# Kernel tuning notes

Hardware: AMD Instinct MI355X
Metric: run time of the kernel (lower is better)

## Reference

```python
import jax, jax.numpy as jnp
import numpy as np

H = 128
NG, NS, NP = 50000, 20000, 30000
NUM_PC_FEATURES = 5
EPS = 1e-12


def seg_sum(x, idx, n):
    return jax.ops.segment_sum(x, idx, num_segments=n)


def seg_mean(x, idx, n):
    s = seg_sum(x, idx, n)
    cnt = seg_sum(jnp.ones((x.shape[0],), x.dtype), idx, n)
    return s / jnp.maximum(cnt, 1.0)[:, None]


def gcn_norm(row, col, n, add_self_loops):
    deg = seg_sum(jnp.ones(row.shape, jnp.float32), col, n)
    if add_self_loops:
        deg = deg + 1.0
    dinv = jnp.where(deg > 0, deg ** -0.5, 0.0)
    return dinv[row] * dinv[col], dinv


def tag_conv(x, row, col, n, Ws, b):
    # TAGConv: out = sum_k (A_hat^k x) W_k + b, symmetric norm, no self loops
    norm, _ = gcn_norm(row, col, n, False)
    out = x @ Ws[0]
    h = x
    for k in range(1, Ws.shape[0]):
        h = seg_sum(norm[:, None] * h[row], col, n)
        out = out + h @ Ws[k]
    return out + b


def rgcn_conv(x, row, col, etype, n, W, root, b):
    # RGCNConv: per-relation mean aggregation + root transform
    h = jnp.einsum('nc,rcd->rnd', x, W)  # [R, N, H]
    msg = h[etype, row]                  # [E, H]
    cnt = jnp.zeros((n, W.shape[0]), x.dtype).at[col, etype].add(1.0)
    w = 1.0 / jnp.maximum(cnt[col, etype], 1.0)
    return seg_sum(msg * w[:, None], col, n) + x @ root + b


def gcn_layer(x, row, col, n, W, b):
    # GCNConv: self loops + symmetric normalization
    xW = x @ W
    norm, dinv = gcn_norm(row, col, n, True)
    return seg_sum(norm[:, None] * xW[row], col, n) + (dinv ** 2)[:, None] * xW + b


def sage_conv(xs, xd, row, col, nd, lw, lb, rw):
    # SAGEConv with mean aggregation, root weight, L2 output normalization
    m = seg_mean(xs[row], col, nd)
    out = m @ lw + lb + xd @ rw
    nrm = jnp.maximum(jnp.linalg.norm(out, axis=-1, keepdims=True), EPS)
    return out / nrm


def setup_inputs() -> dict:
    key = jax.random.key(0)
    ks = iter(jax.random.split(key, 64))

    def nrm(shape):
        return jax.random.normal(next(ks), shape, jnp.float32) * 0.05

    def edges(ns, nd, e):
        return jnp.stack([jax.random.randint(next(ks), (e,), 0, ns, jnp.int32),
                          jax.random.randint(next(ks), (e,), 0, nd, jnp.int32)])

    return dict(
        game_x=nrm((NG, 7)),
        state_x=nrm((NS, 6)),
        pc_x=nrm((NP, NUM_PC_FEATURES)),
        edge_index_v_v=edges(NG, NG, 500000),
        edge_type_v_v=jax.random.randint(next(ks), (500000,), 0, 3, jnp.int32),
        edge_index_history_v_s=edges(NG, NS, 300000),
        edge_attr_history_v_s=nrm((300000, 2)),
        edge_index_in_v_s=edges(NG, NS, 300000),
        edge_index_s_s=edges(NS, NS, 200000),
        edge_index_pc_pc=edges(NP, NP, 300000),
        edge_index_pc_state=edges(NP, NS, 200000),
        edge_index_state_pc=edges(NS, NP, 100000),
        tag10_w=nrm((4, 7, H)), tag10_b=nrm((H,)),
        rgcn_w=nrm((3, H, H)), rgcn_root=nrm((H, H)), rgcn_b=nrm((H,)),
        gcn1_w=nrm((NUM_PC_FEATURES, H)), gcn1_b=nrm((H,)),
        gcn2_w=nrm((H, H)), gcn2_b=nrm((H,)),
        rg_key_w=nrm((6, H)), rg_key_b=nrm((H,)),
        rg_query_w=nrm((H, H)), rg_query_b=nrm((H,)),
        rg_value_w=nrm((H, H)), rg_value_b=nrm((H,)),
        rg_edge_w=nrm((2, H)), rg_skip_w=nrm((6, H)), rg_b=nrm((H,)),
        sage32_lw=nrm((H, H)), sage32_lb=nrm((H,)), sage32_rw=nrm((H, H)),
        sage4_lw=nrm((H, H)), sage4_lb=nrm((H,)), sage4_rw=nrm((H, H)),
        sage42_lw=nrm((H, H)), sage42_lb=nrm((H,)), sage42_rw=nrm((H, H)),
        pcs_lw=nrm((H, H)), pcs_lb=nrm((H,)), pcs_rw=nrm((H, H)),
        tag2_w=nrm((3, H, H)), tag2_b=nrm((H,)),
        sage5_lw=nrm((H, H)), sage5_lb=nrm((H,)), sage5_rw=nrm((H, H)),
        lin_w=nrm((H, 32)), lin_b=nrm((32,)),
        linl_w=nrm((32, 1)), linl_b=nrm((1,)),
    )


def reference(game_x, state_x, pc_x, edge_index_v_v, edge_type_v_v,
              edge_index_history_v_s, edge_attr_history_v_s, edge_index_in_v_s,
              edge_index_s_s, edge_index_pc_pc, edge_index_pc_state, edge_index_state_pc,
              tag10_w, tag10_b, rgcn_w, rgcn_root, rgcn_b,
              gcn1_w, gcn1_b, gcn2_w, gcn2_b,
              rg_key_w, rg_key_b, rg_query_w, rg_query_b, rg_value_w, rg_value_b,
              rg_edge_w, rg_skip_w, rg_b,
              sage32_lw, sage32_lb, sage32_rw,
              sage4_lw, sage4_lb, sage4_rw,
              sage42_lw, sage42_lb, sage42_rw,
              pcs_lw, pcs_lb, pcs_rw,
              tag2_w, tag2_b,
              sage5_lw, sage5_lb, sage5_rw,
              lin_w, lin_b, linl_w, linl_b):
    relu = jax.nn.relu
    rvv, cvv = edge_index_v_v[0], edge_index_v_v[1]
    g = relu(tag_conv(game_x, rvv, cvv, NG, tag10_w, tag10_b))
    g = relu(rgcn_conv(g, rvv, cvv, edge_type_v_v, NG, rgcn_w, rgcn_root, rgcn_b))
    rp, cp = edge_index_pc_pc[0], edge_index_pc_pc[1]
    p = relu(gcn_layer(pc_x, rp, cp, NP, gcn1_w, gcn1_b))
    p = relu(gcn_layer(p, rp, cp, NP, gcn2_w, gcn2_b))
    rh, ch = edge_index_history_v_s[0], edge_index_history_v_s[1]
    # ResGatedGraphConv((game, state), H, edge_dim=2)
    kk = state_x @ rg_key_w + rg_key_b
    q = g @ rg_query_w + rg_query_b
    v = g @ rg_value_w + rg_value_b
    e = edge_attr_history_v_s @ rg_edge_w
    eta = jax.nn.sigmoid(kk[ch] + q[rh] + e)
    s = relu(seg_sum(eta * v[rh], ch, NS) + state_x @ rg_skip_w + rg_b)
    s = relu(sage_conv(g, s, rh, ch, NS, sage32_lw, sage32_lb, sage32_rw))
    ri, ci = edge_index_in_v_s[0], edge_index_in_v_s[1]
    s = relu(sage_conv(g, s, ri, ci, NS, sage4_lw, sage4_lb, sage4_rw))
    s = relu(sage_conv(g, s, ri, ci, NS, sage42_lw, sage42_lb, sage42_rw))
    rps, cps = edge_index_pc_state[0], edge_index_pc_state[1]
    s = relu(sage_conv(p, s, rps, cps, NS, pcs_lw, pcs_lb, pcs_rw))
    rs, cs = edge_index_s_s[0], edge_index_s_s[1]
    s = relu(tag_conv(s, rs, cs, NS, tag2_w, tag2_b))
    s = relu(sage_conv(s, s, rs, cs, NS, sage5_lw, sage5_lb, sage5_rw))
    s = relu(s @ lin_w + lin_b)
    return jax.nn.log_softmax(s @ linl_w + linl_b, axis=0)
```

## Files before the change

kernel.cpp:

```cpp
#include <hip/hip_runtime.h>
#include <cstdint>

#define H 128
static const int NG = 50000, NS = 20000, NP = 30000;

#define TG_RELU 2
#define TG_NORM 4
#define TG_OUTBF16 8

#define CSR_CHUNK 8192

typedef __attribute__((ext_vector_type(8))) short bf16x8;
typedef __attribute__((ext_vector_type(4))) float f32x4;
typedef __attribute__((ext_vector_type(2))) float v2f;

static inline int nblk(long long n) { return (int)((n + 255) / 256); }

__device__ inline unsigned short f2b(float f) {
  unsigned int u = __float_as_uint(f);
  u += 0x7FFFu + ((u >> 16) & 1u);
  return (unsigned short)(u >> 16);
}
__device__ inline float b2f(unsigned short u) {
  return __uint_as_float(((unsigned int)u) << 16);
}
__device__ inline float2 bfp2(unsigned int u) {
  return make_float2(__uint_as_float(u << 16), __uint_as_float(u & 0xFFFF0000u));
}
__device__ inline unsigned int f2bfp(float x, float y) {
  return ((unsigned int)f2b(y) << 16) | (unsigned int)f2b(x);
}
__device__ inline float2 f8p2(unsigned short u) {
  v2f r = __builtin_amdgcn_cvt_pk_f32_fp8((int)(unsigned int)u, false);
  return make_float2(r.x, r.y);
}
__device__ inline unsigned char f2f8(float x) {
  int r = __builtin_amdgcn_cvt_pk_fp8_f32(x, 0.f, 0, false);
  return (unsigned char)(r & 0xFF);
}

struct Seg6 {
  const int* col[6];
  const int* row[6];
  const int* et0;
  int nodeoff[7];
  int edgeoff[7];
  int mode[6];
  float addself[6];
  int hasdinv[6];
};

__global__ __launch_bounds__(256) void k_hist(Seg6 sg, int EE, int* __restrict__ table) {
  __shared__ int h[512];
  int tid = threadIdx.x, blk = blockIdx.x;
  h[tid] = 0; h[tid + 256] = 0;
  __syncthreads();
  int e0 = blk * CSR_CHUNK, e1 = min(EE, e0 + CSR_CHUNK);
  for (int e = e0 + tid; e < e1; e += 256) {
    int gi = 0;
    while (e >= sg.edgeoff[gi + 1]) gi++;
    int le = e - sg.edgeoff[gi];
    int gn = sg.nodeoff[gi] + sg.col[gi][le];
    atomicAdd(&h[gn >> 9], 1);
  }
  __syncthreads();
  table[blk * 512 + tid] = h[tid];
  table[blk * 512 + tid + 256] = h[tid + 256];
}

__global__ void k_scanT(int* __restrict__ table, int nblkA, int* __restrict__ coarseOff) {
  int b = threadIdx.x;
  int s = 0;
  for (int k = 0; k < nblkA; k++) s += table[k * 512 + b];
  __shared__ int cs[512];
  cs[b] = s;
  __syncthreads();
  for (int off = 1; off < 512; off <<= 1) {
    int v = cs[b];
    int u = (b >= off) ? cs[b - off] : 0;
    __syncthreads();
    cs[b] = v + u;
    __syncthreads();
  }
  int excl = (b > 0) ? cs[b - 1] : 0;
  coarseOff[b] = excl;
  if (b == 511) coarseOff[512] = cs[511];
  int run = excl;
  for (int k = 0; k < nblkA; k++) {
    int t = table[k * 512 + b];
    table[k * 512 + b] = run;
    run += t;
  }
}

__global__ __launch_bounds__(256) void k_scatterA(Seg6 sg, int EE, const int* __restrict__ table,
                                                  uint2* __restrict__ tmp) {
  __shared__ int cur[512];
  int tid = threadIdx.x, blk = blockIdx.x;
  cur[tid] = table[blk * 512 + tid];
  cur[tid + 256] = table[blk * 512 + tid + 256];
  __syncthreads();
  int e0 = blk * CSR_CHUNK, e1 = min(EE, e0 + CSR_CHUNK);
  for (int e = e0 + tid; e < e1; e += 256) {
    int gi = 0;
    while (e >= sg.edgeoff[gi + 1]) gi++;
    int le = e - sg.edgeoff[gi];
    int gn = sg.nodeoff[gi] + sg.col[gi][le];
    int m = sg.mode[gi];
    int pay;
    if (m == 2) pay = le;
    else {
      pay = sg.row[gi][le];
      if (m == 1) pay |= sg.et0[le] << 16;
    }
    int pos = atomicAdd(&cur[gn >> 9], 1);
    tmp[pos] = make_uint2((unsigned)gn, (unsigned)pay);
  }
}

__global__ __launch_bounds__(256) void k_localCSR(const uint2* __restrict__ tmp,
                                                  const int* __restrict__ coarseOff,
                                                  Seg6 sg, int NN, int EE, int B,
                                                  int* __restrict__ rowptr,
                                                  int* __restrict__ eidx,
                                                  float* __restrict__ dinv) {
  int b = blockIdx.x, tid = threadIdx.x;
  int base = b * 512;
  int nNodes = min(512, NN - base);
  int beg = coarseOff[b], end = coarseOff[b + 1];
  __shared__ int cnt[512];
  __shared__ int off[512];
  __shared__ int ps[256];
  cnt[tid] = 0; cnt[tid + 256] = 0;
  __syncthreads();
  for (int j = beg + tid; j < end; j += 256)
    atomicAdd(&cnt[tmp[j].x - base], 1);
  __syncthreads();
  int a = cnt[2 * tid], bb = cnt[2 * tid + 1];
  ps[tid] = a + bb;
  __syncthreads();
  for (int o = 1; o < 256; o <<= 1) {
    int v = ps[tid];
    int u = (tid >= o) ? ps[tid - o] : 0;
    __syncthreads();
    ps[tid] = v + u;
    __syncthreads();
  }
  int excl = (tid > 0) ? ps[tid - 1] : 0;
  off[2 * tid] = excl;
  off[2 * tid + 1] = excl + a;
  __syncthreads();
  for (int i = tid; i < nNodes; i += 256) {
    int gid = base + i;
    rowptr[gid] = beg + off[i];
    int gi = 0;
    while (gid >= sg.nodeoff[gi + 1]) gi++;
    if (sg.hasdinv[gi]) {
      float d = (float)cnt[i] + sg.addself[gi];
      dinv[gid] = (d > 0.f) ? rsqrtf(d) : 0.f;
    }
  }
  if (b == B - 1 && tid == 0) rowptr[NN] = EE;
  __syncthreads();
  for (int j = beg + tid; j < end; j += 256) {
    uint2 p = tmp[j];
    int pos = beg + atomicAdd(&off[p.x - base], 1);
    eidx[pos] = (int)p.y;
  }
}

struct PackD { const float* src; int Ksrc; int Kdst; };
struct Pack17 { PackD d[17]; int koff[18]; };

__global__ void k_pack(Pack17 p, unsigned short* __restrict__ Wt, int totalRows) {
  int t = blockIdx.x * blockDim.x + threadIdx.x;
  if (t >= totalRows * 128) return;
  int gk = t >> 7, n = t & 127;
  int w = 0;
  while (gk >= p.koff[w + 1]) w++;
  int k = gk - p.koff[w];
  float v = (k < p.d[w].Ksrc) ? p.d[w].src[(size_t)k * 128 + n] : 0.f;
  Wt[(size_t)p.koff[w] * 128 + (size_t)n * p.d[w].Kdst + k] = f2b(v);
}

__global__ __launch_bounds__(256) void k_gmean(const unsigned short* __restrict__ src,
                                               const int* __restrict__ eidx,
                                               const int* __restrict__ rowptr,
                                               unsigned short* __restrict__ out, int N) {
  int c = blockIdx.x * 4 + (threadIdx.x >> 6);
  if (c >= N) return;
  int lane = threadIdx.x & 63;
  int beg = rowptr[c], end = rowptr[c + 1];
  float2 A0 = {0.f, 0.f}, A1 = {0.f, 0.f}, A2 = {0.f, 0.f}, A3 = {0.f, 0.f};
  int j = beg;
  for (; j + 4 <= end; j += 4) {
    int e0 = eidx[j], e1 = eidx[j + 1], e2 = eidx[j + 2], e3 = eidx[j + 3];
    float2 v0 = bfp2(*(const unsigned int*)(src + (size_t)e0 * H + lane * 2));
    float2 v1 = bfp2(*(const unsigned int*)(src + (size_t)e1 * H + lane * 2));
    float2 v2 = bfp2(*(const unsigned int*)(src + (size_t)e2 * H + lane * 2));
    float2 v3 = bfp2(*(const unsigned int*)(src + (size_t)e3 * H + lane * 2));
    A0.x += v0.x; A0.y += v0.y;
    A1.x += v1.x; A1.y += v1.y;
    A2.x += v2.x; A2.y += v2.y;
    A3.x += v3.x; A3.y += v3.y;
  }
  for (; j < end; j++) {
    float2 v = bfp2(*(const unsigned int*)(src + (size_t)eidx[j] * H + lane * 2));
    A0.x += v.x; A0.y += v.y;
  }
  int cnt = end - beg;
  float s = 1.f / (float)(cnt > 0 ? cnt : 1);
  float ox = (A0.x + A1.x + A2.x + A3.x) * s;
  float oy = (A0.y + A1.y + A2.y + A3.y) * s;
  *(unsigned int*)(out + (size_t)c * H + lane * 2) = f2bfp(ox, oy);
}

__global__ __launch_bounds__(256) void k_gmean_f8(const unsigned char* __restrict__ src,
                                                  const int* __restrict__ eidx,
                                                  const int* __restrict__ rowptr,
                                                  unsigned short* __restrict__ out, int N) {
  int c = blockIdx.x * 4 + (threadIdx.x >> 6);
  if (c >= N) return;
  int lane = threadIdx.x & 63;
  int beg = rowptr[c], end = rowptr[c + 1];
  float2 A0 = {0.f, 0.f}, A1 = {0.f, 0.f}, A2 = {0.f, 0.f}, A3 = {0.f, 0.f};
  int j = beg;
  for (; j + 4 <= end; j += 4) {
    int e0 = eidx[j], e1 = eidx[j + 1], e2 = eidx[j + 2], e3 = eidx[j + 3];
    float2 v0 = f8p2(*(const unsigned short*)(src + (size_t)e0 * H + lane * 2));
    float2 v1 = f8p2(*(const unsigned short*)(src + (size_t)e1 * H + lane * 2));
    float2 v2 = f8p2(*(const unsigned short*)(src + (size_t)e2 * H + lane * 2));
    float2 v3 = f8p2(*(const unsigned short*)(src + (size_t)e3 * H + lane * 2));
    A0.x += v0.x; A0.y += v0.y;
    A1.x += v1.x; A1.y += v1.y;
    A2.x += v2.x; A2.y += v2.y;
    A3.x += v3.x; A3.y += v3.y;
  }
  for (; j < end; j++) {
    float2 v = f8p2(*(const unsigned short*)(src + (size_t)eidx[j] * H + lane * 2));
    A0.x += v.x; A0.y += v.y;
  }
  int cnt = end - beg;
  float s = 1.f / (float)(cnt > 0 ? cnt : 1);
  float ox = (A0.x + A1.x + A2.x + A3.x) * s;
  float oy = (A0.y + A1.y + A2.y + A3.y) * s;
  *(unsigned int*)(out + (size_t)c * H + lane * 2) = f2bfp(ox, oy);
}

__global__ __launch_bounds__(256) void k_grel3(const unsigned char* __restrict__ src,
                                               const int* __restrict__ eidx,
                                               const int* __restrict__ rowptr,
                                               unsigned short* __restrict__ G3, int N) {
  int c = blockIdx.x * 4 + (threadIdx.x >> 6);
  if (c >= N) return;
  int lane = threadIdx.x & 63;
  int beg = rowptr[c], end = rowptr[c + 1];
  float2 a0 = {0.f, 0.f}, a1 = {0.f, 0.f}, a2 = {0.f, 0.f};
  int c0 = 0, c1 = 0, c2 = 0;
  for (int j = beg; j < end; j++) {
    int pk = eidx[j];
    int rel = pk >> 16;
    float2 v = f8p2(*(const unsigned short*)(src + (size_t)(pk & 0xFFFF) * H + lane * 2));
    if (rel == 0) { a0.x += v.x; a0.y += v.y; c0++; }
    else if (rel == 1) { a1.x += v.x; a1.y += v.y; c1++; }
    else { a2.x += v.x; a2.y += v.y; c2++; }
  }
  float s0 = 1.f / (float)(c0 > 0 ? c0 : 1);
  float s1 = 1.f / (float)(c1 > 0 ? c1 : 1);
  float s2 = 1.f / (float)(c2 > 0 ? c2 : 1);
  size_t base = (size_t)c * 384 + lane * 2;
  *(unsigned int*)(G3 + base) = f2bfp(a0.x * s0, a0.y * s0);
  *(unsigned int*)(G3 + base + 128) = f2bfp(a1.x * s1, a1.y * s1);
  *(unsigned int*)(G3 + base + 256) = f2bfp(a2.x * s2, a2.y * s2);
}

__global__ __launch_bounds__(256) void k_gnorm(const unsigned short* __restrict__ src,
                                               long ldS, int offS,
                                               const int* __restrict__ eidx,
                                               const int* __restrict__ rowptr,
                                               const float* __restrict__ dinv,
                                               const unsigned short* __restrict__ selfX,
                                               const float* __restrict__ bias,
                                               unsigned short* __restrict__ out,
                                               long ldD, int offD, int relu, int N) {
  int c = blockIdx.x * 4 + (threadIdx.x >> 6);
  if (c >= N) return;
  int lane = threadIdx.x & 63;
  int beg = rowptr[c], end = rowptr[c + 1];
  float2 A0 = {0.f, 0.f}, A1 = {0.f, 0.f}, A2 = {0.f, 0.f}, A3 = {0.f, 0.f};
  int j = beg;
  for (; j + 4 <= end; j += 4) {
    int e0 = eidx[j], e1 = eidx[j + 1], e2 = eidx[j + 2], e3 = eidx[j + 3];
    float w0 = dinv[e0], w1 = dinv[e1], w2 = dinv[e2], w3 = dinv[e3];
    float2 v0 = bfp2(*(const unsigned int*)(src + (size_t)e0 * ldS + offS + lane * 2));
    float2 v1 = bfp2(*(const unsigned int*)(src + (size_t)e1 * ldS + offS + lane * 2));
    float2 v2 = bfp2(*(const unsigned int*)(src + (size_t)e2 * ldS + offS + lane * 2));
    float2 v3 = bfp2(*(const unsigned int*)(src + (size_t)e3 * ldS + offS + lane * 2));
    A0.x = fmaf(w0, v0.x, A0.x); A0.y = fmaf(w0, v0.y, A0.y);
    A1.x = fmaf(w1, v1.x, A1.x); A1.y = fmaf(w1, v1.y, A1.y);
    A2.x = fmaf(w2, v2.x, A2.x); A2.y = fmaf(w2, v2.y, A2.y);
    A3.x = fmaf(w3, v3.x, A3.x); A3.y = fmaf(w3, v3.y, A3.y);
  }
  for (; j < end; j++) {
    int e = eidx[j];
    float w = dinv[e];
    float2 v = bfp2(*(const unsigned int*)(src + (size_t)e * ldS + offS + lane * 2));
    A0.x = fmaf(w, v.x, A0.x); A0.y = fmaf(w, v.y, A0.y);
  }
  float dc = dinv[c];
  float ox = (A0.x + A1.x + A2.x + A3.x) * dc;
  float oy = (A0.y + A1.y + A2.y + A3.y) * dc;
  if (selfX) {
    float2 sv = bfp2(*(const unsigned int*)(selfX + (size_t)c * H + lane * 2));
    ox += dc * dc * sv.x;
    oy += dc * dc * sv.y;
  }
  if (bias) {
    float2 bv = *(const float2*)(bias + lane * 2);
    ox += bv.x; oy += bv.y;
  }
  if (relu) { ox = fmaxf(ox, 0.f); oy = fmaxf(oy, 0.f); }
  *(unsigned int*)(out + (size_t)c * ldD + offD + lane * 2) = f2bfp(ox, oy);
}

__global__ __launch_bounds__(256) void k_resgated_mean(const unsigned short* __restrict__ kk,
                                                       const unsigned char* __restrict__ q,
                                                       const unsigned char* __restrict__ v,
                                                       const unsigned char* __restrict__ g,
                                                       const float* __restrict__ ea,
                                                       const float* __restrict__ We,
                                                       const int* __restrict__ rh,
                                                       const int* __restrict__ eidx,
                                                       const int* __restrict__ rowptr,
                                                       const float* __restrict__ sx,
                                                       const float* __restrict__ Wsk,
                                                       const float* __restrict__ rgb,
                                                       unsigned short* __restrict__ outS,
                                                       unsigned short* __restrict__ outM, int N) {
  int c = blockIdx.x * 4 + (threadIdx.x >> 6);
  if (c >= N) return;
  int lane = threadIdx.x & 63;
  int d0 = lane * 2;
  int beg = rowptr[c], end = rowptr[c + 1];
  float2 kload = bfp2(*(const unsigned int*)(kk + (size_t)c * H + d0));
  float2 we0 = make_float2(We[d0], We[d0 + 1]);
  float2 we1 = make_float2(We[H + d0], We[H + d0 + 1]);
  float2 accS = {0.f, 0.f}, accM = {0.f, 0.f};
  for (int j = beg; j < end; j++) {
    int e = eidx[j];
    int r = rh[e];
    float a0 = ea[2 * e], a1 = ea[2 * e + 1];
    float2 qv = f8p2(*(const unsigned short*)(q + (size_t)r * H + d0));
    float2 vv = f8p2(*(const unsigned short*)(v + (size_t)r * H + d0));
    float2 gv = f8p2(*(const unsigned short*)(g + (size_t)r * H + d0));
    float x0 = kload.x + qv.x + a0 * we0.x + a1 * we1.x;
    float x1 = kload.y + qv.y + a0 * we0.y + a1 * we1.y;
    float eta0 = 1.f / (1.f + __expf(-x0));
    float eta1 = 1.f / (1.f + __expf(-x1));
    accS.x = fmaf(eta0, vv.x, accS.x);
    accS.y = fmaf(eta1, vv.y, accS.y);
    accM.x += gv.x; accM.y += gv.y;
  }
  float sk0 = rgb[d0], sk1 = rgb[d0 + 1];
#pragma unroll
  for (int f = 0; f < 6; f++) {
    float xf = sx[c * 6 + f];
    sk0 = fmaf(xf, Wsk[f * H + d0], sk0);
    sk1 = fmaf(xf, Wsk[f * H + d0 + 1], sk1);
  }
  *(unsigned int*)(outS + (size_t)c * H + d0) =
      f2bfp(fmaxf(accS.x + sk0, 0.f), fmaxf(accS.y + sk1, 0.f));
  int cnt = end - beg;
  float s = 1.f / (float)(cnt > 0 ? cnt : 1);
  *(unsigned int*)(outM + (size_t)c * H + d0) = f2bfp(accM.x * s, accM.y * s);
}

__global__ void k_gather_norm7(const unsigned short* __restrict__ src, int ldS, int offS,
                               const int* __restrict__ eidx, const int* __restrict__ rowptr,
                               const float* __restrict__ dinv, unsigned short* __restrict__ dst,
                               int ldD, int offD) {
  int c = blockIdx.x;
  int t = threadIdx.x;
  int f = t & 7, j = t >> 3;
  int beg = rowptr[c], end = rowptr[c + 1];
  __shared__ int si[64];
  __shared__ float sw[64];
  __shared__ float red[8][8];
  float acc = 0.f;
  for (int j0 = beg; j0 < end; j0 += 64) {
    int nn = min(64, end - j0);
    __syncthreads();
    if (t < nn) {
      int r = eidx[j0 + t] & 0xFFFF;
      si[t] = r;
      sw[t] = dinv[r];
    }
    __syncthreads();
    if (f < 7)
      for (int u = j; u < nn; u += 8) acc += sw[u] * b2f(src[(size_t)si[u] * ldS + offS + f]);
  }
  red[j][f] = acc;
  __syncthreads();
  if (j == 0 && f < 7) {
    float s = 0.f;
    for (int u = 0; u < 8; u++) s += red[u][f];
    dst[(size_t)c * ldD + offD + f] = f2b(s * dinv[c]);
  }
}

__global__ void k_copy7b(const float* __restrict__ src, unsigned short* __restrict__ dst, int n) {
  long long t = (long long)blockIdx.x * blockDim.x + threadIdx.x;
  int i = (int)(t >> 3), f = (int)(t & 7);
  if (i < n && f < 7) dst[(size_t)i * 32 + f] = f2b(src[(size_t)i * 7 + f]);
}

__global__ void k_gemm128b(const float* __restrict__ X, const float* __restrict__ W,
                           const float* __restrict__ b, unsigned short* __restrict__ out,
                           int M, int K) {
  long long t = (long long)blockIdx.x * blockDim.x + threadIdx.x;
  if (t >= (long long)M * H) return;
  int i = (int)(t >> 7), h = (int)(t & 127);
  float acc = b ? b[h] : 0.f;
  const float* x = X + (long long)i * K;
  for (int k = 0; k < K; k++) acc = fmaf(x[k], W[k * H + h], acc);
  out[t] = f2b(acc);
}

__global__ __launch_bounds__(256) void k_mgemm(const unsigned short* __restrict__ X1, int ldX1, int K1,
                                               const unsigned short* __restrict__ W1t,
                                               const unsigned short* __restrict__ X2, int ldX2, int K2,
                                               const unsigned short* __restrict__ W2t,
                                               const float* __restrict__ bias,
                                               void* __restrict__ Cv, long ldC,
                                               int M, int flags,
                                               unsigned char* __restrict__ C8) {
  __shared__ unsigned short Als[64 * 40];
  __shared__ unsigned short Bls[128 * 40];
  __shared__ float rs[2][64];
  int tid = threadIdx.x;
  int lane = tid & 63, wv = tid >> 6;
  int m = lane & 15, q = lane >> 4;
  int rbase = (wv & 1) * 32;
  int cbase = (wv >> 1) * 64;
  int blockRow = blockIdx.x * 64;
  int sr = tid >> 2, skc = (tid & 3) * 8;
  f32x4 acc[2][4];
#pragma unroll
  for (int a = 0; a < 2; a++)
#pragma unroll
    for (int b = 0; b < 4; b++) acc[a][b] = (f32x4){0.f, 0.f, 0.f, 0.f};

  int Ktot = K1 + K2;
  for (int k0 = 0; k0 < Ktot; k0 += 32) {
    const unsigned short* Xb;
    const unsigned short* Wt_;
    int kr, ldx, Kw;
    if (k0 < K1) { Xb = X1; Wt_ = W1t; kr = k0; ldx = ldX1; Kw = K1; }
    else { Xb = X2; Wt_ = W2t; kr = k0 - K1; ldx = ldX2; Kw = K2; }
    __syncthreads();
    {
      int gr = blockRow + sr;
      bf16x8 xv = (bf16x8){0, 0, 0, 0, 0, 0, 0, 0};
      if (gr < M) xv = *(const bf16x8*)(Xb + (size_t)gr * ldx + kr + skc);
      *(bf16x8*)&Als[sr * 40 + skc] = xv;
    }
#pragma unroll
    for (int it = 0; it < 2; it++) {
      int fid = it * 256 + tid;
      int n = fid >> 2, kc = (fid & 3) * 8;
      *(bf16x8*)&Bls[n * 40 + kc] = *(const bf16x8*)(Wt_ + (size_t)n * Kw + kr + kc);
    }
    __syncthreads();
    bf16x8 a0 = *(const bf16x8*)&Als[(rbase + m) * 40 + q * 8];
    bf16x8 a1 = *(const bf16x8*)&Als[(rbase + 16 + m) * 40 + q * 8];
    bf16x8 b0 = *(const bf16x8*)&Bls[(cbase + m) * 40 + q * 8];
    bf16x8 b1 = *(const bf16x8*)&Bls[(cbase + 16 + m) * 40 + q * 8];
    bf16x8 b2 = *(const bf16x8*)&Bls[(cbase + 32 + m) * 40 + q * 8];
    bf16x8 b3 = *(const bf16x8*)&Bls[(cbase + 48 + m) * 40 + q * 8];
    acc[0][0] = __builtin_amdgcn_mfma_f32_16x16x32_bf16(a0, b0, acc[0][0], 0, 0, 0);
    acc[0][1] = __builtin_amdgcn_mfma_f32_16x16x32_bf16(a0, b1, acc[0][1], 0, 0, 0);
    acc[0][2] = __builtin_amdgcn_mfma_f32_16x16x32_bf16(a0, b2, acc[0][2], 0, 0, 0);
    acc[0][3] = __builtin_amdgcn_mfma_f32_16x16x32_bf16(a0, b3, acc[0][3], 0, 0, 0);
    acc[1][0] = __builtin_amdgcn_mfma_f32_16x16x32_bf16(a1, b0, acc[1][0], 0, 0, 0);
    acc[1][1] = __builtin_amdgcn_mfma_f32_16x16x32_bf16(a1, b1, acc[1][1], 0, 0, 0);
    acc[1][2] = __builtin_amdgcn_mfma_f32_16x16x32_bf16(a1, b2, acc[1][2], 0, 0, 0);
    acc[1][3] = __builtin_amdgcn_mfma_f32_16x16x32_bf16(a1, b3, acc[1][3], 0, 0, 0);
  }
  float ov[2][4][4];
  float bcol[4] = {0.f, 0.f, 0.f, 0.f};
  if (bias) {
#pragma unroll
    for (int j = 0; j < 4; j++) bcol[j] = bias[cbase + j * 16 + m];
  }
#pragma unroll
  for (int a = 0; a < 2; a++)
#pragma unroll
    for (int j = 0; j < 4; j++)
#pragma unroll
      for (int i = 0; i < 4; i++) ov[a][j][i] = acc[a][j][i] + bcol[j];

  if (flags & TG_NORM) {
#pragma unroll
    for (int a = 0; a < 2; a++)
#pragma unroll
      for (int i = 0; i < 4; i++) {
        float p = 0.f;
#pragma unroll
        for (int j = 0; j < 4; j++) p = fmaf(ov[a][j][i], ov[a][j][i], p);
        p += __shfl_xor(p, 1);
        p += __shfl_xor(p, 2);
        p += __shfl_xor(p, 4);
        p += __shfl_xor(p, 8);
        if (m == 0) rs[wv >> 1][rbase + a * 16 + q * 4 + i] = p;
      }
    __syncthreads();
#pragma unroll
    for (int a = 0; a < 2; a++)
#pragma unroll
      for (int i = 0; i < 4; i++) {
        int ridx = rbase + a * 16 + q * 4 + i;
        float s = rs[0][ridx] + rs[1][ridx];
        float f = 1.f / fmaxf(sqrtf(s), 1e-12f);
#pragma unroll
        for (int j = 0; j < 4; j++) ov[a][j][i] = fmaxf(ov[a][j][i] * f, 0.f);
      }
  } else if (flags & TG_RELU) {
#pragma unroll
    for (int a = 0; a < 2; a++)
#pragma unroll
      for (int j = 0; j < 4; j++)
#pragma unroll
        for (int i = 0; i < 4; i++) ov[a][j][i] = fmaxf(ov[a][j][i], 0.f);
  }
  if (flags & TG_OUTBF16) {
    unsigned short* C = (unsigned short*)Cv;
#pragma unroll
    for (int a = 0; a < 2; a++)
#pragma unroll
      for (int i = 0; i < 4; i++) {
        int row = blockRow + rbase + a * 16 + q * 4 + i;
        if (row < M) {
#pragma unroll
          for (int j = 0; j < 4; j++)
            C[(size_t)row * ldC + cbase + j * 16 + m] = f2b(ov[a][j][i]);
        }
      }
  } else {
    float* C = (float*)Cv;
#pragma unroll
    for (int a = 0; a < 2; a++)
#pragma unroll
      for (int i = 0; i < 4; i++) {
        int row = blockRow + rbase + a * 16 + q * 4 + i;
        if (row < M) {
#pragma unroll
          for (int j = 0; j < 4; j++)
            C[(size_t)row * ldC + cbase + j * 16 + m] = ov[a][j][i];
        }
      }
  }
  if (C8) {
#pragma unroll
    for (int a = 0; a < 2; a++)
#pragma unroll
      for (int i = 0; i < 4; i++) {
        int row = blockRow + rbase + a * 16 + q * 4 + i;
        if (row < M) {
#pragma unroll
          for (int j = 0; j < 4; j++)
            C8[(size_t)row * ldC + cbase + j * 16 + m] = f2f8(ov[a][j][i]);
        }
      }
  }
}

static inline int mgb(int M) { return (M + 63) / 64; }

__global__ __launch_bounds__(256) void k_head(const float* __restrict__ X,
                                              const float* __restrict__ lw,
                                              const float* __restrict__ lb,
                                              const float* __restrict__ lwl,
                                              const float* __restrict__ lbl,
                                              float* __restrict__ z, int M) {
  __shared__ float Wl[128 * 32];
  __shared__ float Xs[8][128];
  int tid = threadIdx.x;
  for (int i = tid * 4; i < 4096; i += 1024) *(float4*)&Wl[i] = *(const float4*)&lw[i];
  int rowBase = blockIdx.x * 8;
  {
    int idx = tid * 4;
    int xr = idx >> 7, xc = idx & 127;
    int grow = rowBase + xr;
    float4 v = make_float4(0.f, 0.f, 0.f, 0.f);
    if (grow < M) v = *(const float4*)(X + (size_t)grow * H + xc);
    *(float4*)&Xs[xr][xc] = v;
  }
  __syncthreads();
  int r = tid >> 5, o = tid & 31;
  float acc = lb[o];
  for (int k = 0; k < 128; k++) acc = fmaf(Xs[r][k], Wl[k * 32 + o], acc);
  acc = fmaxf(acc, 0.f) * lwl[o];
  for (int s = 16; s > 0; s >>= 1) acc += __shfl_down(acc, s, 32);
  int grow = rowBase + r;
  if (o == 0 && grow < M) z[grow] = acc + lbl[0];
}

__global__ void k_logsoftmax(const float* __restrict__ z, float* __restrict__ out, int n) {
  __shared__ float red[256];
  int tid = threadIdx.x;
  float m = -1e30f;
  for (int i = tid; i < n; i += 256) m = fmaxf(m, z[i]);
  red[tid] = m;
  __syncthreads();
  for (int s = 128; s > 0; s >>= 1) {
    if (tid < s) red[tid] = fmaxf(red[tid], red[tid + s]);
    __syncthreads();
  }
  float mx = red[0];
  __syncthreads();
  float sum = 0.f;
  for (int i = tid; i < n; i += 256) sum += __expf(z[i] - mx);
  red[tid] = sum;
  __syncthreads();
  for (int s = 128; s > 0; s >>= 1) {
    if (tid < s) red[tid] += red[tid + s];
    __syncthreads();
  }
  float lse = mx + logf(red[0]);
  for (int i = tid; i < n; i += 256) out[i] = z[i] - lse;
}

extern "C" void kernel_launch(void* const* d_in, const int* in_sizes, int n_in,
                              void* d_out, int out_size, void* d_ws, size_t ws_size,
                              hipStream_t stream) {
  const float* game_x = (const float*)d_in[0];
  const float* state_x = (const float*)d_in[1];
  const float* pc_x = (const float*)d_in[2];
  const int* ei_vv = (const int*)d_in[3];
  const int* et_vv = (const int*)d_in[4];
  const int* ei_hist = (const int*)d_in[5];
  const float* ea_hist = (const float*)d_in[6];
  const int* ei_in = (const int*)d_in[7];
  const int* ei_ss = (const int*)d_in[8];
  const int* ei_pp = (const int*)d_in[9];
  const int* ei_ps = (const int*)d_in[10];
  const float* tag10_w = (const float*)d_in[12];
  const float* tag10_b = (const float*)d_in[13];
  const float* rgcn_w = (const float*)d_in[14];
  const float* rgcn_root = (const float*)d_in[15];
  const float* rgcn_b = (const float*)d_in[16];
  const float* gcn1_w = (const float*)d_in[17];
  const float* gcn1_b = (const float*)d_in[18];
  const float* gcn2_w = (const float*)d_in[19];
  const float* gcn2_b = (const float*)d_in[20];
  const float* rg_key_w = (const float*)d_in[21];
  const float* rg_key_b = (const float*)d_in[22];
  const float* rg_query_w = (const float*)d_in[23];
  const float* rg_query_b = (const float*)d_in[24];
  const float* rg_value_w = (const float*)d_in[25];
  const float* rg_value_b = (const float*)d_in[26];
  const float* rg_edge_w = (const float*)d_in[27];
  const float* rg_skip_w = (const float*)d_in[28];
  const float* rg_b = (const float*)d_in[29];
  const float* sage32_lw = (const float*)d_in[30];
  const float* sage32_lb = (const float*)d_in[31];
  const float* sage32_rw = (const float*)d_in[32];
  const float* sage4_lw = (const float*)d_in[33];
  const float* sage4_lb = (const float*)d_in[34];
  const float* sage4_rw = (const float*)d_in[35];
  const float* sage42_lw = (const float*)d_in[36];
  const float* sage42_lb = (const float*)d_in[37];
  const float* sage42_rw = (const float*)d_in[38];
  const float* pcs_lw = (const float*)d_in[39];
  const float* pcs_lb = (const float*)d_in[40];
  const float* pcs_rw = (const float*)d_in[41];
  const float* tag2_w = (const float*)d_in[42];
  const float* tag2_b = (const float*)d_in[43];
  const float* sage5_lw = (const float*)d_in[44];
  const float* sage5_lb = (const float*)d_in[45];
  const float* sage5_rw = (const float*)d_in[46];
  const float* lin_w = (const float*)d_in[47];
  const float* lin_b = (const float*)d_in[48];
  const float* linl_w = (const float*)d_in[49];
  const float* linl_b = (const float*)d_in[50];

  const int Evv = in_sizes[3] / 2, Eh = in_sizes[5] / 2, Ein = in_sizes[7] / 2,
            Ess = in_sizes[8] / 2, Epp = in_sizes[9] / 2, Eps = in_sizes[10] / 2;
  const int EE = Evv + Epp + Eh + Ein + Eps + Ess;
  const int NN = NG + NP + 4 * NS;

  char* base = (char*)d_ws;
  const size_t B_NGH = (size_t)NG * H * 2;
  const size_t B_NPH = (size_t)NP * H * 2;
  const size_t B_NSH = (size_t)NS * H * 2;
  unsigned short* g_tag_b = (unsigned short*)base;
  unsigned short* g_b = (unsigned short*)(base + B_NGH);
  char* C0 = base + 2 * B_NGH;
  uint2* tmp_pairs = (uint2*)C0;
  unsigned short* P_tag10_b = (unsigned short*)C0;
  unsigned short* G3_b = (unsigned short*)C0;
  unsigned short* xW_b = (unsigned short*)C0;
  unsigned short* p1b_b = (unsigned short*)(C0 + B_NPH);
  unsigned short* p2b_b = (unsigned short*)(C0 + 2 * B_NPH);
  unsigned short* v_b = (unsigned short*)C0;
  unsigned short* q_b = g_tag_b;
  unsigned short* P_tag2_b = (unsigned short*)C0;
  char* S0 = base + 2 * B_NGH + 46000000;
  unsigned short* S_a_b = (unsigned short*)S0;
  unsigned short* S_b_b = (unsigned short*)(S0 + B_NSH);
  unsigned short* m_buf_b = (unsigned short*)(S0 + 2 * B_NSH);
  unsigned short* kk_b = (unsigned short*)(S0 + 3 * B_NSH);
  float* Sfin = (float*)(S0 + 4 * B_NSH);
  unsigned short* Wt = (unsigned short*)(S0 + 4 * B_NSH + (size_t)NS * H * 4);
  int* ip = (int*)(S0 + 4 * B_NSH + (size_t)NS * H * 4 + 700000);
  int* rp_all = ip; ip += NN + 1;
  int* eidx_all = ip; ip += EE;
  int* table = ip; ip += 512 * 240;
  int* coarseOff = ip; ip += 520;
  float* fp = (float*)ip;
  float* dinv_all = fp; fp += NN;
  float* z = fp; fp += NS;
  unsigned char* g_tag_8 = (unsigned char*)(z + NS);
  unsigned char* g_8 = g_tag_8 + (size_t)NG * H;
  unsigned char* q_8 = g_8 + (size_t)NG * H;
  unsigned char* v_8 = q_8 + (size_t)NG * H;

  Seg6 sg;
  sg.col[0] = ei_vv + Evv;  sg.row[0] = ei_vv;
  sg.col[1] = ei_pp + Epp;  sg.row[1] = ei_pp;
  sg.col[2] = ei_hist + Eh; sg.row[2] = ei_hist;
  sg.col[3] = ei_in + Ein;  sg.row[3] = ei_in;
  sg.col[4] = ei_ps + Eps;  sg.row[4] = ei_ps;
  sg.col[5] = ei_ss + Ess;  sg.row[5] = ei_ss;
  sg.et0 = et_vv;
  int no[7] = {0, NG, NG + NP, NG + NP + NS, NG + NP + 2 * NS, NG + NP + 3 * NS, NN};
  int eo[7] = {0, Evv, Evv + Epp, Evv + Epp + Eh, Evv + Epp + Eh + Ein,
               Evv + Epp + Eh + Ein + Eps, EE};
  for (int i = 0; i < 7; i++) { sg.nodeoff[i] = no[i]; sg.edgeoff[i] = eo[i]; }
  int md[6] = {1, 0, 2, 0, 0, 0};
  float as[6] = {0.f, 1.f, 0.f, 0.f, 0.f, 0.f};
  int hd[6] = {1, 1, 0, 0, 0, 1};
  for (int i = 0; i < 6; i++) { sg.mode[i] = md[i]; sg.addself[i] = as[i]; sg.hasdinv[i] = hd[i]; }

  const int* rp_vv = rp_all + no[0];
  const int* rp_pp = rp_all + no[1];
  const int* rp_hh = rp_all + no[2];
  const int* rp_in = rp_all + no[3];
  const int* rp_ps = rp_all + no[4];
  const int* rp_ss = rp_all + no[5];
  const float* dinvG = dinv_all + no[0];
  const float* dinvP = dinv_all + no[1];
  const float* dinvS = dinv_all + no[5];
  const int* rh = ei_hist;

  Pack17 pk;
  const float* wsrc[17] = {tag10_w, rgcn_w, rgcn_root, gcn2_w, rg_query_w, rg_value_w,
                           sage32_lw, sage32_rw, sage4_lw, sage4_rw, sage42_lw, sage42_rw,
                           pcs_lw, pcs_rw, tag2_w, sage5_lw, sage5_rw};
  int ksrc[17] = {28, 384, 128, 128, 128, 128, 128, 128, 128, 128, 128, 128, 128, 128, 384, 128, 128};
  int kdst[17] = {32, 384, 128, 128, 128, 128, 128, 128, 128, 128, 128, 128, 128, 128, 384, 128, 128};
  int run = 0;
  for (int i = 0; i < 17; i++) {
    pk.d[i].src = wsrc[i]; pk.d[i].Ksrc = ksrc[i]; pk.d[i].Kdst = kdst[i];
    pk.koff[i] = run; run += kdst[i];
  }
  pk.koff[17] = run;
  unsigned short* WT[17];
  for (int i = 0; i < 17; i++) WT[i] = Wt + (size_t)pk.koff[i] * 128;
  k_pack<<<nblk((long long)run * 128), 256, 0, stream>>>(pk, Wt, run);

  int nblkA = (EE + CSR_CHUNK - 1) / CSR_CHUNK;
  int B = (NN + 511) / 512;
  k_hist<<<nblkA, 256, 0, stream>>>(sg, EE, table);
  k_scanT<<<1, 512, 0, stream>>>(table, nblkA, coarseOff);
  k_scatterA<<<nblkA, 256, 0, stream>>>(sg, EE, table, tmp_pairs);
  k_localCSR<<<B, 256, 0, stream>>>(tmp_pairs, coarseOff, sg, NN, EE, B,
                                    rp_all, eidx_all, dinv_all);

  hipMemsetAsync(P_tag10_b, 0, (size_t)NG * 32 * 2, stream);
  k_copy7b<<<nblk((long long)NG * 8), 256, 0, stream>>>(game_x, P_tag10_b, NG);
  k_gather_norm7<<<NG, 64, 0, stream>>>(P_tag10_b, 32, 0, eidx_all, rp_vv, dinvG, P_tag10_b, 32, 7);
  k_gather_norm7<<<NG, 64, 0, stream>>>(P_tag10_b, 32, 7, eidx_all, rp_vv, dinvG, P_tag10_b, 32, 14);
  k_gather_norm7<<<NG, 64, 0, stream>>>(P_tag10_b, 32, 14, eidx_all, rp_vv, dinvG, P_tag10_b, 32, 21);
  k_mgemm<<<mgb(NG), 256, 0, stream>>>(P_tag10_b, 32, 32, WT[0], nullptr, 0, 0, nullptr,
                                       tag10_b, g_tag_b, H, NG, TG_RELU | TG_OUTBF16, g_tag_8);

  k_grel3<<<(NG + 3) / 4, 256, 0, stream>>>(g_tag_8, eidx_all, rp_vv, G3_b, NG);
  k_mgemm<<<mgb(NG), 256, 0, stream>>>(G3_b, 384, 384, WT[1], g_tag_b, H, H, WT[2],
                                       rgcn_b, g_b, H, NG, TG_RELU | TG_OUTBF16, g_8);

  k_gemm128b<<<nblk((long long)NP * H), 256, 0, stream>>>(pc_x, gcn1_w, nullptr, xW_b, NP, 5);
  k_gnorm<<<(NP + 3) / 4, 256, 0, stream>>>(xW_b, H, 0, eidx_all, rp_pp, dinvP, xW_b, gcn1_b,
                                            p1b_b, H, 0, 1, NP);
  k_mgemm<<<mgb(NP), 256, 0, stream>>>(p1b_b, H, H, WT[3], nullptr, 0, 0, nullptr,
                                       nullptr, xW_b, H, NP, TG_OUTBF16, nullptr);
  k_gnorm<<<(NP + 3) / 4, 256, 0, stream>>>(xW_b, H, 0, eidx_all, rp_pp, dinvP, xW_b, gcn2_b,
                                            p2b_b, H, 0, 1, NP);

  k_gemm128b<<<nblk((long long)NS * H), 256, 0, stream>>>(state_x, rg_key_w, rg_key_b, kk_b, NS, 6);
  k_mgemm<<<mgb(NG), 256, 0, stream>>>(g_b, H, H, WT[4], nullptr, 0, 0, nullptr,
                                       rg_query_b, q_b, H, NG, TG_OUTBF16, q_8);
  k_mgemm<<<mgb(NG), 256, 0, stream>>>(g_b, H, H, WT[5], nullptr, 0, 0, nullptr,
                                       rg_value_b, v_b, H, NG, TG_OUTBF16, v_8);
  k_resgated_mean<<<(NS + 3) / 4, 256, 0, stream>>>(kk_b, q_8, v_8, g_8, ea_hist, rg_edge_w, rh,
                                                    eidx_all, rp_hh, state_x, rg_skip_w, rg_b,
                                                    S_a_b, m_buf_b, NS);

  k_mgemm<<<mgb(NS), 256, 0, stream>>>(m_buf_b, H, H, WT[6], S_a_b, H, H, WT[7],
                                       sage32_lb, S_b_b, H, NS, TG_NORM | TG_OUTBF16, nullptr);

  k_gmean_f8<<<(NS + 3) / 4, 256, 0, stream>>>(g_8, eidx_all, rp_in, m_buf_b, NS);
  k_mgemm<<<mgb(NS), 256, 0, stream>>>(m_buf_b, H, H, WT[8], S_b_b, H, H, WT[9],
                                       sage4_lb, S_a_b, H, NS, TG_NORM | TG_OUTBF16, nullptr);
  k_mgemm<<<mgb(NS), 256, 0, stream>>>(m_buf_b, H, H, WT[10], S_a_b, H, H, WT[11],
                                       sage42_lb, S_b_b, H, NS, TG_NORM | TG_OUTBF16, nullptr);

  k_gmean<<<(NS + 3) / 4, 256, 0, stream>>>(p2b_b, eidx_all, rp_ps, m_buf_b, NS);
  k_mgemm<<<mgb(NS), 256, 0, stream>>>(m_buf_b, H, H, WT[12], S_b_b, H, H, WT[13],
                                       pcs_lb, P_tag2_b, 384, NS, TG_NORM | TG_OUTBF16, nullptr);

  k_gnorm<<<(NS + 3) / 4, 256, 0, stream>>>(P_tag2_b, 384, 0, eidx_all, rp_ss, dinvS, nullptr,
                                            nullptr, P_tag2_b, 384, 128, 0, NS);
  k_gnorm<<<(NS + 3) / 4, 256, 0, stream>>>(P_tag2_b, 384, 128, eidx_all, rp_ss, dinvS, nullptr,
                                            nullptr, P_tag2_b, 384, 256, 0, NS);
  k_mgemm<<<mgb(NS), 256, 0, stream>>>(P_tag2_b, 384, 384, WT[14], nullptr, 0, 0, nullptr,
                                       tag2_b, S_b_b, H, NS, TG_RELU | TG_OUTBF16, nullptr);

  k_gmean<<<(NS + 3) / 4, 256, 0, stream>>>(S_b_b, eidx_all, rp_ss, m_buf_b, NS);
  k_mgemm<<<mgb(NS), 256, 0, stream>>>(m_buf_b, H, H, WT[15], S_b_b, H, H, WT[16],
                                       sage5_lb, Sfin, H, NS, TG_NORM, nullptr);

  k_head<<<(NS + 7) / 8, 256, 0, stream>>>(Sfin, lin_w, lin_b, linl_w, linl_b, z, NS);
  k_logsoftmax<<<1, 256, 0, stream>>>(z, (float*)d_out, NS);
}
```

Measured before the change: 806.9 us.

## Unroll gather loops by four and use wave-per-node 7-wide TAG gather

```diff
diff --git a/kernel.cpp b/kernel.cpp
--- a/kernel.cpp
+++ b/kernel.cpp
@@ -257,7 +257,28 @@
   int beg = rowptr[c], end = rowptr[c + 1];
   float2 a0 = {0.f, 0.f}, a1 = {0.f, 0.f}, a2 = {0.f, 0.f};
   int c0 = 0, c1 = 0, c2 = 0;
-  for (int j = beg; j < end; j++) {
+  int j = beg;
+  for (; j + 4 <= end; j += 4) {
+    int p0 = eidx[j], p1 = eidx[j + 1], p2 = eidx[j + 2], p3 = eidx[j + 3];
+    float2 w0 = f8p2(*(const unsigned short*)(src + (size_t)(p0 & 0xFFFF) * H + lane * 2));
+    float2 w1 = f8p2(*(const unsigned short*)(src + (size_t)(p1 & 0xFFFF) * H + lane * 2));
+    float2 w2 = f8p2(*(const unsigned short*)(src + (size_t)(p2 & 0xFFFF) * H + lane * 2));
+    float2 w3 = f8p2(*(const unsigned short*)(src + (size_t)(p3 & 0xFFFF) * H + lane * 2));
+    int r0 = p0 >> 16, r1 = p1 >> 16, r2 = p2 >> 16, r3 = p3 >> 16;
+    if (r0 == 0) { a0.x += w0.x; a0.y += w0.y; c0++; }
+    else if (r0 == 1) { a1.x += w0.x; a1.y += w0.y; c1++; }
+    else { a2.x += w0.x; a2.y += w0.y; c2++; }
+    if (r1 == 0) { a0.x += w1.x; a0.y += w1.y; c0++; }
+    else if (r1 == 1) { a1.x += w1.x; a1.y += w1.y; c1++; }
+    else { a2.x += w1.x; a2.y += w1.y; c2++; }
+    if (r2 == 0) { a0.x += w2.x; a0.y += w2.y; c0++; }
+    else if (r2 == 1) { a1.x += w2.x; a1.y += w2.y; c1++; }
+    else { a2.x += w2.x; a2.y += w2.y; c2++; }
+    if (r3 == 0) { a0.x += w3.x; a0.y += w3.y; c0++; }
+    else if (r3 == 1) { a1.x += w3.x; a1.y += w3.y; c1++; }
+    else { a2.x += w3.x; a2.y += w3.y; c2++; }
+  }
+  for (; j < end; j++) {
     int pk = eidx[j];
     int rel = pk >> 16;
     float2 v = f8p2(*(const unsigned short*)(src + (size_t)(pk & 0xFFFF) * H + lane * 2));
@@ -346,21 +367,54 @@
   float2 we0 = make_float2(We[d0], We[d0 + 1]);
   float2 we1 = make_float2(We[H + d0], We[H + d0 + 1]);
   float2 accS = {0.f, 0.f}, accM = {0.f, 0.f};
-  for (int j = beg; j < end; j++) {
+  int j = beg;
+  for (; j + 4 <= end; j += 4) {
+    int e0 = eidx[j], e1 = eidx[j + 1], e2 = eidx[j + 2], e3 = eidx[j + 3];
+    int r0 = rh[e0], r1 = rh[e1], r2 = rh[e2], r3 = rh[e3];
+    float2 ea0 = *(const float2*)(ea + 2 * e0);
+    float2 ea1 = *(const float2*)(ea + 2 * e1);
+    float2 ea2 = *(const float2*)(ea + 2 * e2);
+    float2 ea3 = *(const float2*)(ea + 2 * e3);
+    unsigned short uq0 = *(const unsigned short*)(q + (size_t)r0 * H + d0);
+    unsigned short uv0 = *(const unsigned short*)(v + (size_t)r0 * H + d0);
+    unsigned short ug0 = *(const unsigned short*)(g + (size_t)r0 * H + d0);
+    unsigned short uq1 = *(const unsigned short*)(q + (size_t)r1 * H + d0);
+    unsigned short uv1 = *(const unsigned short*)(v + (size_t)r1 * H + d0);
+    unsigned short ug1 = *(const unsigned short*)(g + (size_t)r1 * H + d0);
+    unsigned short uq2 = *(const unsigned short*)(q + (size_t)r2 * H + d0);
+    unsigned short uv2 = *(const unsigned short*)(v + (size_t)r2 * H + d0);
+    unsigned short ug2 = *(const unsigned short*)(g + (size_t)r2 * H + d0);
+    unsigned short uq3 = *(const unsigned short*)(q + (size_t)r3 * H + d0);
+    unsigned short uv3 = *(const unsigned short*)(v + (size_t)r3 * H + d0);
+    unsigned short ug3 = *(const unsigned short*)(g + (size_t)r3 * H + d0);
+#define RG_STEP(UQ, UV, UG, EA)                                            \
+    {                                                                      \
+      float2 qv = f8p2(UQ);                                                \
+      float2 vv = f8p2(UV);                                                \
+      float2 gv = f8p2(UG);                                                \
+      float x0 = kload.x + qv.x + (EA).x * we0.x + (EA).y * we1.x;         \
+      float x1 = kload.y + qv.y + (EA).x * we0.y + (EA).y * we1.y;         \
+      float eta0 = 1.f / (1.f + __expf(-x0));                              \
+      float eta1 = 1.f / (1.f + __expf(-x1));                              \
+      accS.x = fmaf(eta0, vv.x, accS.x);                                   \
+      accS.y = fmaf(eta1, vv.y, accS.y);                                   \
+      accM.x += gv.x; accM.y += gv.y;                                      \
+    }
+    RG_STEP(uq0, uv0, ug0, ea0)
+    RG_STEP(uq1, uv1, ug1, ea1)
+    RG_STEP(uq2, uv2, ug2, ea2)
+    RG_STEP(uq3, uv3, ug3, ea3)
+  }
+  for (; j < end; j++) {
     int e = eidx[j];
     int r = rh[e];
-    float a0 = ea[2 * e], a1 = ea[2 * e + 1];
-    float2 qv = f8p2(*(const unsigned short*)(q + (size_t)r * H + d0));
-    float2 vv = f8p2(*(const unsigned short*)(v + (size_t)r * H + d0));
-    float2 gv = f8p2(*(const unsigned short*)(g + (size_t)r * H + d0));
-    float x0 = kload.x + qv.x + a0 * we0.x + a1 * we1.x;
-    float x1 = kload.y + qv.y + a0 * we0.y + a1 * we1.y;
-    float eta0 = 1.f / (1.f + __expf(-x0));
-    float eta1 = 1.f / (1.f + __expf(-x1));
-    accS.x = fmaf(eta0, vv.x, accS.x);
-    accS.y = fmaf(eta1, vv.y, accS.y);
-    accM.x += gv.x; accM.y += gv.y;
-  }
+    float2 eav = *(const float2*)(ea + 2 * e);
+    unsigned short uq = *(const unsigned short*)(q + (size_t)r * H + d0);
+    unsigned short uv = *(const unsigned short*)(v + (size_t)r * H + d0);
+    unsigned short ug = *(const unsigned short*)(g + (size_t)r * H + d0);
+    RG_STEP(uq, uv, ug, eav)
+  }
+#undef RG_STEP
   float sk0 = rgb[d0], sk1 = rgb[d0 + 1];
 #pragma unroll
   for (int f = 0; f < 6; f++) {
@@ -375,37 +429,30 @@
   *(unsigned int*)(outM + (size_t)c * H + d0) = f2bfp(accM.x * s, accM.y * s);
 }
 
-__global__ void k_gather_norm7(const unsigned short* __restrict__ src, int ldS, int offS,
-                               const int* __restrict__ eidx, const int* __restrict__ rowptr,
-                               const float* __restrict__ dinv, unsigned short* __restrict__ dst,
-                               int ldD, int offD) {
-  int c = blockIdx.x;
-  int t = threadIdx.x;
-  int f = t & 7, j = t >> 3;
+__global__ __launch_bounds__(256) void k_gnorm7w(const unsigned short* __restrict__ src,
+                                                 int ldS, int offS,
+                                                 const int* __restrict__ eidx,
+                                                 const int* __restrict__ rowptr,
+                                                 const float* __restrict__ dinv,
+                                                 unsigned short* __restrict__ dst,
+                                                 int ldD, int offD, int N) {
+  int c = blockIdx.x * 4 + (threadIdx.x >> 6);
+  if (c >= N) return;
+  int lane = threadIdx.x & 63;
+  int eg = lane >> 3, f = lane & 7;
   int beg = rowptr[c], end = rowptr[c + 1];
-  __shared__ int si[64];
-  __shared__ float sw[64];
-  __shared__ float red[8][8];
   float acc = 0.f;
-  for (int j0 = beg; j0 < end; j0 += 64) {
-    int nn = min(64, end - j0);
-    __syncthreads();
-    if (t < nn) {
-      int r = eidx[j0 + t] & 0xFFFF;
-      si[t] = r;
-      sw[t] = dinv[r];
-    }
-    __syncthreads();
-    if (f < 7)
-      for (int u = j; u < nn; u += 8) acc += sw[u] * b2f(src[(size_t)si[u] * ldS + offS + f]);
-  }
-  red[j][f] = acc;
-  __syncthreads();
-  if (j == 0 && f < 7) {
-    float s = 0.f;
-    for (int u = 0; u < 8; u++) s += red[u][f];
-    dst[(size_t)c * ldD + offD + f] = f2b(s * dinv[c]);
-  }
+  for (int j = beg + eg; j < end; j += 8) {
+    int r = eidx[j] & 0xFFFF;
+    float w = dinv[r];
+    float val = (f < 7) ? b2f(src[(size_t)r * ldS + offS + f]) : 0.f;
+    acc = fmaf(w, val, acc);
+  }
+  acc += __shfl_xor(acc, 8);
+  acc += __shfl_xor(acc, 16);
+  acc += __shfl_xor(acc, 32);
+  if (eg == 0 && f < 7)
+    dst[(size_t)c * ldD + offD + f] = f2b(acc * dinv[c]);
 }
 
 __global__ void k_copy7b(const float* __restrict__ src, unsigned short* __restrict__ dst, int n) {
@@ -779,9 +826,12 @@
 
   hipMemsetAsync(P_tag10_b, 0, (size_t)NG * 32 * 2, stream);
   k_copy7b<<<nblk((long long)NG * 8), 256, 0, stream>>>(game_x, P_tag10_b, NG);
-  k_gather_norm7<<<NG, 64, 0, stream>>>(P_tag10_b, 32, 0, eidx_all, rp_vv, dinvG, P_tag10_b, 32, 7);
-  k_gather_norm7<<<NG, 64, 0, stream>>>(P_tag10_b, 32, 7, eidx_all, rp_vv, dinvG, P_tag10_b, 32, 14);
-  k_gather_norm7<<<NG, 64, 0, stream>>>(P_tag10_b, 32, 14, eidx_all, rp_vv, dinvG, P_tag10_b, 32, 21);
+  k_gnorm7w<<<(NG + 3) / 4, 256, 0, stream>>>(P_tag10_b, 32, 0, eidx_all, rp_vv, dinvG,
+                                              P_tag10_b, 32, 7, NG);
+  k_gnorm7w<<<(NG + 3) / 4, 256, 0, stream>>>(P_tag10_b, 32, 7, eidx_all, rp_vv, dinvG,
+                                              P_tag10_b, 32, 14, NG);
+  k_gnorm7w<<<(NG + 3) / 4, 256, 0, stream>>>(P_tag10_b, 32, 14, eidx_all, rp_vv, dinvG,
+                                              P_tag10_b, 32, 21, NG);
   k_mgemm<<<mgb(NG), 256, 0, stream>>>(P_tag10_b, 32, 32, WT[0], nullptr, 0, 0, nullptr,
                                        tag10_b, g_tag_b, H, NG, TG_RELU | TG_OUTBF16, g_tag_8);
 
```

After: 753.7 us. 6.6% less time.
